# Performance work log

Measured on AMD Instinct MI355X. Metric: run time of the kernel, lower is better.

## Reference

```python
import jax, jax.numpy as jnp
import numpy as np

SEGMENT_LENGTHS = (768, 1536, 3072, 6144, 12288)
DILATED_RATIOS = (1, 2, 4, 8, 16)
NUM_HEADS = 12
NEG_INF = -1e9


def _layer_norm(x, g, b, eps=1e-5):
    mu = jnp.mean(x, axis=-1, keepdims=True)
    var = jnp.mean((x - mu) ** 2, axis=-1, keepdims=True)
    return (x - mu) * jax.lax.rsqrt(var + eps) * g + b


def _dilated_branch(q, k, v, w, r):
    # q,k,v: (B, L, H, Dh); segment length w, dilation ratio r (w % r == 0)
    B, L, H, Dh = q.shape
    Lp = -(-L // w) * w
    n, m = Lp // w, w // r
    gsz = -(-H // r)  # head-group size (heads padded up to a multiple of r in LongNet)
    offs = jnp.arange(H) // gsz  # per-head token offset within each r-block
    oh = jax.nn.one_hot(offs, r, dtype=q.dtype)  # (H, r)

    def gather(t):
        t = jnp.pad(t, ((0, 0), (0, Lp - L), (0, 0), (0, 0)))
        t = t.reshape(B, n, m, r, H, Dh)  # segments of w = m blocks of r
        return jnp.einsum('bnmrhd,hr->bnmhd', t, oh)  # each head picks its offset

    qi, ki, vi = gather(q), gather(k), gather(v)
    s = jnp.einsum('bnihd,bnjhd->bnhij', qi * (Dh ** -0.5), ki)  # (B,n,H,m,m)
    lse = jax.scipy.special.logsumexp(s, axis=-1)  # (B,n,H,m)
    o = jnp.einsum('bnhij,bnjhd->bnihd', jax.nn.softmax(s, axis=-1), vi)
    # scatter back to dense token positions; uncovered slots get 0 / -inf lse
    o_full = jnp.einsum('bnmhd,hr->bnmrhd', o, oh).reshape(B, Lp, H, Dh)
    lse = jnp.transpose(lse, (0, 1, 3, 2))  # (B,n,m,H)
    lse_full = jnp.where(oh.T[None, None, None] > 0, lse[:, :, :, None, :], NEG_INF)
    lse_full = lse_full.reshape(B, Lp, H)
    return o_full[:, :L], lse_full[:, :L]


def _dilated_attention(q, k, v):
    outs, lses = [], []
    for w, r in zip(SEGMENT_LENGTHS, DILATED_RATIOS):
        o, l = _dilated_branch(q, k, v, w, r)
        outs.append(o)
        lses.append(l)
    lse = jnp.stack(lses)  # (n_branch, B, L, H)
    wts = jnp.exp(lse - lse.max(0))
    wts = wts / wts.sum(0)  # softmax-combine branches by their lse (LongNet recombination)
    return (jnp.stack(outs) * wts[..., None]).sum(0)  # (B, L, H, Dh)


def _forward(x, patch_w, patch_b, cls_token, pos_embed,
             ln1_g, ln1_b, wq, bq, wk, bk, wv, bv, wo, bo,
             ln2_g, ln2_b, w1, b1, w2, b2, normf_g, normf_b, head_w, head_b):
    B, Cin, D, Hs, Ws = x.shape
    E = patch_w.shape[0]
    pd, ph, pw = patch_w.shape[2], patch_w.shape[3], patch_w.shape[4]
    # non-overlapping 3D patch embed (Conv3d with stride == kernel)
    xp = x.reshape(B, Cin, D // pd, pd, Hs // ph, ph, Ws // pw, pw)
    tok = jnp.einsum('bcxpyqzr,ecpqr->bxyze', xp, patch_w).reshape(B, -1, E) + patch_b
    tok = tok + pos_embed[:, 1:]
    cls = cls_token + pos_embed[:, :1]
    h = jnp.concatenate([jnp.broadcast_to(cls, (B, 1, E)), tok], axis=1)
    L = h.shape[1]
    Dh = E // NUM_HEADS
    depth = wq.shape[0]
    for i in range(depth):  # pre-LN transformer layers with LongNet dilated attention
        hn = _layer_norm(h, ln1_g[i], ln1_b[i])
        q = (hn @ wq[i] + bq[i]).reshape(B, L, NUM_HEADS, Dh)
        k = (hn @ wk[i] + bk[i]).reshape(B, L, NUM_HEADS, Dh)
        v = (hn @ wv[i] + bv[i]).reshape(B, L, NUM_HEADS, Dh)
        a = _dilated_attention(q, k, v).reshape(B, L, E)
        h = h + a @ wo[i] + bo[i]
        hn = _layer_norm(h, ln2_g[i], ln2_b[i])
        h = h + jax.nn.gelu(hn @ w1[i] + b1[i], approximate=False) @ w2[i] + b2[i]
    h = _layer_norm(h, normf_g, normf_b)
    return h[:, 0] @ head_w + head_b  # (B, num_classes)


def setup_inputs() -> dict:
    key = jax.random.key(0)
    ks = jax.random.split(key, 12)
    B, E, depth, ncls = 2, 768, 2, 1000
    D, Hs, Ws = 48, 256, 256
    N = (D // 4) * (Hs // 16) * (Ws // 16)  # 3072 patches
    f32 = jnp.float32
    s = 0.02
    return {
        'x': jax.random.normal(ks[0], (B, 1, D, Hs, Ws), f32),
        'patch_w': jax.random.normal(ks[1], (E, 1, 4, 16, 16), f32) * s,
        'patch_b': jnp.zeros((E,), f32),
        'cls_token': jax.random.normal(ks[2], (1, 1, E), f32) * s,
        'pos_embed': jax.random.normal(ks[3], (1, N + 1, E), f32) * s,
        'ln1_g': jnp.ones((depth, E), f32),
        'ln1_b': jnp.zeros((depth, E), f32),
        'wq': jax.random.normal(ks[4], (depth, E, E), f32) * s,
        'bq': jnp.zeros((depth, E), f32),
        'wk': jax.random.normal(ks[5], (depth, E, E), f32) * s,
        'bk': jnp.zeros((depth, E), f32),
        'wv': jax.random.normal(ks[6], (depth, E, E), f32) * s,
        'bv': jnp.zeros((depth, E), f32),
        'wo': jax.random.normal(ks[7], (depth, E, E), f32) * s,
        'bo': jnp.zeros((depth, E), f32),
        'ln2_g': jnp.ones((depth, E), f32),
        'ln2_b': jnp.zeros((depth, E), f32),
        'w1': jax.random.normal(ks[8], (depth, E, 4 * E), f32) * s,
        'b1': jnp.zeros((depth, 4 * E), f32),
        'w2': jax.random.normal(ks[9], (depth, 4 * E, E), f32) * s,
        'b2': jnp.zeros((depth, E), f32),
        'normf_g': jnp.ones((E,), f32),
        'normf_b': jnp.zeros((E,), f32),
        'head_w': jax.random.normal(ks[10], (E, ncls), f32) * s,
        'head_b': jnp.zeros((ncls,), f32),
    }


def reference(x, patch_w, patch_b, cls_token, pos_embed,
              ln1_g, ln1_b, wq, bq, wk, bk, wv, bv, wo, bo,
              ln2_g, ln2_b, w1, b1, w2, b2, normf_g, normf_b, head_w, head_b):
    return _forward(x, patch_w, patch_b, cls_token, pos_embed,
                    ln1_g, ln1_b, wq, bq, wk, bk, wv, bv, wo, bo,
                    ln2_g, ln2_b, w1, b1, w2, b2, normf_g, normf_b, head_w, head_b)
```

## Files before the change

kernel.cpp:

```cpp
#include <hip/hip_runtime.h>
#include <math.h>

#define TOK_L 3073
#define EMB 768
#define NH 12
#define DH 64
#define BATCH 2
#define QKVS 2304
#define HSZ ((size_t)BATCH * TOK_L * EMB)
#define MHC ((size_t)BATCH * TOK_L * NH)

typedef __bf16 bf16;
typedef __bf16 v8bf __attribute__((ext_vector_type(8)));
typedef __bf16 v4bf __attribute__((ext_vector_type(4)));
typedef float  v4f  __attribute__((ext_vector_type(4)));
typedef unsigned int v4u __attribute__((ext_vector_type(4)));

__device__ __forceinline__ v8bf zero8() {
    v8bf v;
    #pragma unroll
    for (int i = 0; i < 8; i++) v[i] = (bf16)0.f;
    return v;
}
__device__ __forceinline__ v4f zero4() {
    v4f v; v[0] = 0.f; v[1] = 0.f; v[2] = 0.f; v[3] = 0.f; return v;
}
__device__ __forceinline__ float gelu_f(float x) {
    return 0.5f * x * (1.0f + erff(x * 0.70710678118654752f));
}
__device__ __forceinline__ void gload16(const bf16* g, bf16* l) {
    __builtin_amdgcn_global_load_lds(
        (const __attribute__((address_space(1))) void*)g,
        (__attribute__((address_space(3))) void*)l, 16, 0, 0);
}

__device__ __forceinline__ void convT_tile(const float* __restrict__ src,
                                           bf16* __restrict__ dst,
                                           int K, int N, int tx, int ty)
{
    __shared__ float t[32][33];
    int n0 = tx * 32, k0 = ty * 32;
    int r = threadIdx.x >> 3, c4 = (threadIdx.x & 7) * 4;
    float4 v = *(const float4*)(src + (size_t)(k0 + r) * N + n0 + c4);
    t[r][c4 + 0] = v.x; t[r][c4 + 1] = v.y; t[r][c4 + 2] = v.z; t[r][c4 + 3] = v.w;
    __syncthreads();
    v4bf o;
    o[0] = (bf16)t[c4 + 0][r]; o[1] = (bf16)t[c4 + 1][r];
    o[2] = (bf16)t[c4 + 2][r]; o[3] = (bf16)t[c4 + 3][r];
    *(v4bf*)(dst + (size_t)(n0 + r) * K + k0 + c4) = o;
}

__global__ __launch_bounds__(256) void prep_weights(
    const float* __restrict__ wq, const float* __restrict__ wk,
    const float* __restrict__ wv, const float* __restrict__ wo,
    const float* __restrict__ w1, const float* __restrict__ w2,
    const float* __restrict__ patch_w,
    bf16* __restrict__ qkv_t0, bf16* __restrict__ wo_t0,
    bf16* __restrict__ w1_t, bf16* __restrict__ w2_t, bf16* __restrict__ pw_b)
{
    int bid = blockIdx.x;
    if (bid >= 13824) {
        int i = ((bid - 13824) * 256 + threadIdx.x) * 4;
        float4 v = *(const float4*)(patch_w + i);
        v4bf o; o[0] = (bf16)v.x; o[1] = (bf16)v.y; o[2] = (bf16)v.z; o[3] = (bf16)v.w;
        *(v4bf*)(pw_b + i) = o;
        return;
    }
    int layer = bid / 6912, t = bid % 6912;
    if (t < 1728) {
        int m = t / 576, tt = t % 576;
        const float* src = (m == 0 ? wq : m == 1 ? wk : wv) + (size_t)layer * 589824;
        bf16* dst = qkv_t0 + (size_t)layer * QKVS * 768 + (size_t)m * 589824;
        convT_tile(src, dst, 768, 768, tt % 24, tt / 24);
    } else if (t < 2304) {
        int tt = t - 1728;
        convT_tile(wo + (size_t)layer * 589824, wo_t0 + (size_t)layer * 589824,
                   768, 768, tt % 24, tt / 24);
    } else if (t < 4608) {
        int tt = t - 2304;
        convT_tile(w1 + (size_t)layer * 2359296, w1_t + (size_t)layer * 2359296,
                   768, 3072, tt % 96, tt / 96);
    } else {
        int tt = t - 4608;
        convT_tile(w2 + (size_t)layer * 2359296, w2_t + (size_t)layer * 2359296,
                   3072, 768, tt % 24, tt / 24);
    }
}

__global__ __launch_bounds__(256) void prep_small(const float* __restrict__ bq,
    const float* __restrict__ bk, const float* __restrict__ bv, float* __restrict__ d,
    const float* __restrict__ cls, const float* __restrict__ pos, float* __restrict__ h)
{
    int i = blockIdx.x * 256 + threadIdx.x;
    if (i < 2 * QKVS) {
        int layer = i / QKVS, j = i % QKVS;
        const float* s = (j < 768) ? bq : (j < 1536) ? bk : bv;
        d[i] = s[(size_t)layer * 768 + (j & 767)];
    }
    if (i < 2 * 768) {
        int b = i / 768, e = i % 768;
        h[(size_t)b * TOK_L * EMB + e] = cls[e] + pos[e];
    }
}

__global__ __launch_bounds__(256) void gather_patches(const float* __restrict__ x,
                                                      bf16* __restrict__ Xp) {
    int p = blockIdx.x;
    int b = p / 3072, pp = p % 3072;
    int px = pp >> 8, py = (pp >> 4) & 15, pz = pp & 15;
    for (int k = threadIdx.x; k < 1024; k += 256) {
        int pd = k >> 8, ph = (k >> 4) & 15, pw = k & 15;
        size_t src = ((size_t)(b * 48 + px * 4 + pd)) * 65536
                   + (size_t)(py * 16 + ph) * 256 + (size_t)(pz * 16 + pw);
        Xp[(size_t)p * 1024 + k] = (bf16)x[src];
    }
}

__device__ __forceinline__ void remap_tile(int NX, int MY, int G, int& xo, int& yo)
{
    int id = blockIdx.x + NX * blockIdx.y;
    int nwg = NX * MY;
    int xcd = id & 7, j = id >> 3;
    int q = nwg >> 3, r = nwg & 7;
    int n = xcd * q + (xcd < r ? xcd : r) + j;
    int full = MY / G;
    int bpg = NX * G;
    int nf = full * bpg;
    if (n < nf) {
        int gi = n / bpg, w = n - gi * bpg;
        int xi = w / G;
        xo = xi; yo = gi * G + (w - xi * G);
    } else {
        int t = MY - full * G;
        int w = n - nf;
        int xi = w / t;
        xo = xi; yo = full * G + (w - xi * t);
    }
}

template<int BN>
__global__ __launch_bounds__(256) void gemm_bf16(
    const bf16* __restrict__ A, const bf16* __restrict__ Bt,
    const float* __restrict__ bias, float* __restrict__ Cf,
    bf16* __restrict__ Cb, int M, int N, int K, int flags,
    const float* __restrict__ pos, int G)
{
    __shared__ bf16 As[3][128 * 32];
    __shared__ bf16 Bs[3][BN * 32];
    const int tid = threadIdx.x;
    const int lane = tid & 63, wid = tid >> 6;
    const int ln15 = lane & 15, q4 = lane >> 4;
    int xo, yo;
    remap_tile(gridDim.x, gridDim.y, G, xo, yo);
    const int m0 = yo * 128, n0 = xo * BN;
    const int wm = (wid & 1) * 64, wn = (wid >> 1) * (BN / 2);
    const int srow = lane >> 2;
    const int schunk = (lane & 3) * 8;
    const int NF = BN / 32;

    v4f acc[4][NF];
    #pragma unroll
    for (int i = 0; i < 4; i++)
        #pragma unroll
        for (int j = 0; j < NF; j++) acc[i][j] = zero4();

    const int NT = K >> 5;
    auto stage = [&](int kt, int bi) {
        const int k0 = kt << 5;
        #pragma unroll
        for (int i = 0; i < 2; i++) {
            int rg = wid * 32 + i * 16;
            int gm = m0 + rg + srow; if (gm >= M) gm = M - 1;
            gload16(A + (size_t)gm * K + k0 + schunk, &As[bi][rg * 32]);
        }
        if (BN == 128) {
            #pragma unroll
            for (int i = 0; i < 2; i++) {
                int rg = wid * 32 + i * 16;
                gload16(Bt + (size_t)(n0 + rg + srow) * K + k0 + schunk, &Bs[bi][rg * 32]);
            }
        } else {
            int rg = wid * 16;
            gload16(Bt + (size_t)(n0 + rg + srow) * K + k0 + schunk, &Bs[bi][rg * 32]);
        }
    };

    stage(0, 0);
    if (NT > 1) stage(1, 1);

    int cur = 0;
    for (int kt = 0; kt < NT; kt++) {
        int nx2 = cur + 2; if (nx2 >= 3) nx2 -= 3;
        if (kt + 2 < NT) {
            stage(kt + 2, nx2);
            if (BN == 128) asm volatile("s_waitcnt vmcnt(8)" ::: "memory");
            else           asm volatile("s_waitcnt vmcnt(6)" ::: "memory");
        } else if (kt + 1 < NT) {
            if (BN == 128) asm volatile("s_waitcnt vmcnt(4)" ::: "memory");
            else           asm volatile("s_waitcnt vmcnt(3)" ::: "memory");
        } else {
            asm volatile("s_waitcnt vmcnt(0)" ::: "memory");
        }
        __builtin_amdgcn_sched_barrier(0);
        __builtin_amdgcn_s_barrier();

        v8bf af[4], bfr[NF];
        #pragma unroll
        for (int mt = 0; mt < 4; mt++)
            af[mt] = *(const v8bf*)(&As[cur][(wm + mt * 16 + ln15) * 32 + q4 * 8]);
        #pragma unroll
        for (int nt = 0; nt < NF; nt++)
            bfr[nt] = *(const v8bf*)(&Bs[cur][(wn + nt * 16 + ln15) * 32 + q4 * 8]);
        #pragma unroll
        for (int mt = 0; mt < 4; mt++)
            #pragma unroll
            for (int nt = 0; nt < NF; nt++)
                acc[mt][nt] = __builtin_amdgcn_mfma_f32_16x16x32_bf16(af[mt], bfr[nt], acc[mt][nt], 0, 0, 0);
        __builtin_amdgcn_s_barrier();
        cur = cur + 1 == 3 ? 0 : cur + 1;
    }
    #pragma unroll
    for (int mt = 0; mt < 4; mt++) {
        #pragma unroll
        for (int nt = 0; nt < NF; nt++) {
            #pragma unroll
            for (int g = 0; g < 4; g++) {
                int row = m0 + wm + mt * 16 + q4 * 4 + g;
                if (row >= M) continue;
                int col = n0 + wn + nt * 16 + ln15;
                float v = acc[mt][nt][g] + bias[col];
                if (flags & 2) v = gelu_f(v);
                size_t crow;
                if (flags & 4) {
                    int rowp = row % 3072;
                    crow = (size_t)(row + row / 3072 + 1);
                    v += pos[(size_t)(rowp + 1) * EMB + col];
                } else crow = (size_t)row;
                size_t ci = crow * (size_t)N + col;
                if (flags & 8) Cb[ci] = (bf16)v;
                else { if (flags & 1) v += Cf[ci]; Cf[ci] = v; }
            }
        }
    }
}

__global__ __launch_bounds__(256) void layernorm_kernel(
    const float* __restrict__ x, const float* __restrict__ g,
    const float* __restrict__ bb, bf16* __restrict__ y, int nrows)
{
    int row = blockIdx.x;
    if (row >= nrows) return;
    int tid = threadIdx.x;
    const float* xr = x + (size_t)row * EMB;
    float v0 = xr[tid], v1 = xr[tid + 256], v2 = xr[tid + 512];
    __shared__ float red[256];
    red[tid] = v0 + v1 + v2;
    __syncthreads();
    for (int o = 128; o > 0; o >>= 1) { if (tid < o) red[tid] += red[tid + o]; __syncthreads(); }
    float mu = red[0] * (1.f / 768.f);
    __syncthreads();
    float d0 = v0 - mu, d1 = v1 - mu, d2 = v2 - mu;
    red[tid] = d0 * d0 + d1 * d1 + d2 * d2;
    __syncthreads();
    for (int o = 128; o > 0; o >>= 1) { if (tid < o) red[tid] += red[tid + o]; __syncthreads(); }
    float rs = rsqrtf(red[0] * (1.f / 768.f) + 1e-5f);
    bf16* yr = y + (size_t)row * EMB;
    yr[tid]       = (bf16)(d0 * rs * g[tid]       + bb[tid]);
    yr[tid + 256] = (bf16)(d1 * rs * g[tid + 256] + bb[tid + 256]);
    yr[tid + 512] = (bf16)(d2 * rs * g[tid + 512] + bb[tid + 512]);
}

__global__ __launch_bounds__(256) void pack_vt(const bf16* __restrict__ qkv,
                                               bf16* __restrict__ Vt)
{
    __shared__ bf16 t[64 * 65];
    int yy = blockIdx.y;
    int br, seg;
    if (yy < 5)       { br = 0; seg = yy; }
    else if (yy < 8)  { br = 1; seg = yy - 5; }
    else if (yy < 10) { br = 2; seg = yy - 8; }
    else if (yy == 10){ br = 3; seg = 0; }
    else              { br = 4; seg = 0; }
    const int r = 1 << br, w = 768 << br;
    const int gsz = (NH + r - 1) / r;
    const int bh = blockIdx.z;
    const int b = bh / NH, hd = bh % NH;
    const int off = hd / gsz;
    const int kbase = seg * w + off;
    const int kt = blockIdx.x;
    const int tid = threadIdx.x;
    const int dq = (tid & 7) * 8;
    #pragma unroll
    for (int p = 0; p < 2; p++) {
        int jl = (tid >> 3) + p * 32;
        int pk = kbase + (kt * 64 + jl) * r;
        v8bf val = (pk < TOK_L)
            ? *(const v8bf*)(qkv + (size_t)(b * TOK_L + pk) * QKVS + 1536 + hd * DH + dq)
            : zero8();
        #pragma unroll
        for (int i = 0; i < 8; i++) t[jl * 65 + dq + i] = val[i];
    }
    __syncthreads();
    #pragma unroll
    for (int p = 0; p < 2; p++) {
        int d = (tid >> 3) + p * 32;
        int kk = (tid & 7) * 8;
        v8bf o;
        #pragma unroll
        for (int i = 0; i < 8; i++) o[i] = t[(kk + i) * 65 + d];
        *(v8bf*)(Vt + ((size_t)(yy * 24 + bh) * 64 + d) * 768 + kt * 64 + kk) = o;
    }
}

__global__ __launch_bounds__(256) void attn_mfma(
    const bf16* __restrict__ qkv, const bf16* __restrict__ Vt,
    bf16* __restrict__ oac, bf16* __restrict__ obr, float* __restrict__ lse5)
{
    __shared__ bf16 kl[2 * 4096];
    const int tid = threadIdx.x;
    const int lane = tid & 63, wid = tid >> 6;
    const int ln15 = lane & 15, q4 = lane >> 4;
    const int bid = blockIdx.x;
    const int xcd = bid & 7, rest = bid >> 3;
    const int slot = rest / 6, t = rest - slot * 6;
    const int g = (slot << 3) | xcd;
    const int yy = g / 24, bh = g - yy * 24;
    int br, seg;
    if (yy < 5)       { br = 0; seg = yy; }
    else if (yy < 8)  { br = 1; seg = yy - 5; }
    else if (yy < 10) { br = 2; seg = yy - 8; }
    else if (yy == 10){ br = 3; seg = 0; }
    else              { br = 4; seg = 0; }
    const int r = 1 << br, w = 768 << br;
    const int gsz = (NH + r - 1) / r;
    const int b = bh / NH, hd = bh % NH;
    const int off = hd / gsz;
    const int sbase = seg * w + off;
    if (sbase + (t * 128) * r >= TOK_L) return;

    int n_valid = (TOK_L - sbase + r - 1) / r;
    if (n_valid > 768) n_valid = 768;
    const int kt_lim = (n_valid + 63) >> 6;
    const float pad_add = (float)(768 - n_valid);
    const int qoff = t * 128 + wid * 32;
    const bool wactive = (sbase + qoff * r) < TOK_L;

    const bf16* qb_ = qkv + hd * DH;
    const bf16* kb_ = qkv + 768 + hd * DH;

    const int swz = (ln15 & 7) * 8;

    auto stageK = [&](int ktv, int bufi) {
        #pragma unroll
        for (int p = 0; p < 2; p++) {
            int row = (tid >> 3) + p * 32;
            int pk = sbase + (ktv * 64 + row) * r;
            if (pk >= TOK_L) pk = 0;
            int colsw = ((tid & 7) ^ ((tid >> 3) & 7)) * 8;
            gload16(kb_ + (size_t)(b * TOK_L + pk) * QKVS + colsw,
                    kl + bufi * 4096 + wid * 512 + p * 2048);
        }
    };

    v8bf qf[2][2];
    #pragma unroll
    for (int mt = 0; mt < 2; mt++) {
        int pq = sbase + (qoff + mt * 16 + ln15) * r;
        #pragma unroll
        for (int ks = 0; ks < 2; ks++) {
            v8bf qv = (pq < TOK_L)
                ? *(const v8bf*)(qb_ + (size_t)(b * TOK_L + pq) * QKVS + ks * 32 + q4 * 8)
                : zero8();
            #pragma unroll
            for (int i = 0; i < 8; i++) qv[i] = (bf16)((float)qv[i] * 0.125f);
            qf[mt][ks] = qv;
        }
    }
    v4f o[2][4];
    float lsum[2];
    #pragma unroll
    for (int mt = 0; mt < 2; mt++) {
        lsum[mt] = 0.f;
        #pragma unroll
        for (int dt = 0; dt < 4; dt++) o[mt][dt] = zero4();
    }

    const bf16* vtb = Vt + (size_t)(yy * 24 + bh) * 64 * 768;

    stageK(0, 0);
    __syncthreads();

    for (int kt = 0; kt < kt_lim; kt++) {
        const int cur = kt & 1;
        if (kt + 1 < kt_lim) stageK(kt + 1, cur ^ 1);
        if (wactive) {
            const bf16* klc = kl + cur * 4096;
            v8bf kf[4][2];
            #pragma unroll
            for (int nt = 0; nt < 4; nt++)
                #pragma unroll
                for (int ks = 0; ks < 2; ks++)
                    kf[nt][ks] = *(const v8bf*)(klc + (nt * 16 + ln15) * 64
                                                + ((ks * 32 + q4 * 8) ^ swz));
            unsigned int paw[2][2][4];
            #pragma unroll
            for (int mt = 0; mt < 2; mt++) {
                v4f s[4];
                #pragma unroll
                for (int nt = 0; nt < 4; nt++) {
                    s[nt] = __builtin_amdgcn_mfma_f32_16x16x32_bf16(kf[nt][0], qf[mt][0], zero4(), 0, 0, 0);
                    s[nt] = __builtin_amdgcn_mfma_f32_16x16x32_bf16(kf[nt][1], qf[mt][1], s[nt], 0, 0, 0);
                }
                unsigned int W[4][2];
                float ls = 0.f;
                #pragma unroll
                for (int nt = 0; nt < 4; nt++) {
                    int kb = kt * 64 + nt * 16 + q4 * 4;
                    float p0 = (kb + 0 < n_valid) ? __expf(s[nt][0]) : 0.f;
                    float p1 = (kb + 1 < n_valid) ? __expf(s[nt][1]) : 0.f;
                    float p2 = (kb + 2 < n_valid) ? __expf(s[nt][2]) : 0.f;
                    float p3 = (kb + 3 < n_valid) ? __expf(s[nt][3]) : 0.f;
                    ls += (p0 + p1) + (p2 + p3);
                    asm("v_cvt_pk_bf16_f32 %0, %1, %2" : "=v"(W[nt][0]) : "v"(p0), "v"(p1));
                    asm("v_cvt_pk_bf16_f32 %0, %1, %2" : "=v"(W[nt][1]) : "v"(p2), "v"(p3));
                }
                lsum[mt] += ls;
                #pragma unroll
                for (int ks = 0; ks < 2; ks++) {
                    #pragma unroll
                    for (int h = 0; h < 2; h++) {
                        unsigned int a = W[2 * ks][h], c = W[2 * ks + 1][h];
                        asm("v_permlane32_swap_b32 %0, %1" : "+v"(a), "+v"(c));
                        asm("v_permlane16_swap_b32 %0, %1" : "+v"(a), "+v"(c));
                        paw[mt][ks][h]     = a;
                        paw[mt][ks][2 + h] = c;
                    }
                }
            }
            #pragma unroll
            for (int ks = 0; ks < 2; ks++) {
                v8bf vf[4];
                #pragma unroll
                for (int dt = 0; dt < 4; dt++)
                    vf[dt] = *(const v8bf*)(vtb + (size_t)(dt * 16 + ln15) * 768 + kt * 64 + ks * 32 + q4 * 8);
                #pragma unroll
                for (int mt = 0; mt < 2; mt++) {
                    v4u pw = { paw[mt][ks][0], paw[mt][ks][1], paw[mt][ks][2], paw[mt][ks][3] };
                    v8bf pa = __builtin_bit_cast(v8bf, pw);
                    #pragma unroll
                    for (int dt = 0; dt < 4; dt++)
                        o[mt][dt] = __builtin_amdgcn_mfma_f32_16x16x32_bf16(pa, vf[dt], o[mt][dt], 0, 0, 0);
                }
            }
        }
        __syncthreads();
    }
    if (!wactive) return;

    float lf[2];
    #pragma unroll
    for (int mt = 0; mt < 2; mt++) {
        float l = lsum[mt];
        l += __shfl_xor(l, 16, 64);
        l += __shfl_xor(l, 32, 64);
        l += pad_add;
        lf[mt] = l;
        if (q4 == 0) {
            int pq = sbase + (qoff + mt * 16 + ln15) * r;
            if (pq < TOK_L)
                lse5[(size_t)br * MHC + (size_t)(b * TOK_L + pq) * NH + hd] = __logf(l);
        }
    }

    bf16* od = (br == 0) ? oac : obr + (size_t)(br - 1) * HSZ;
    #pragma unroll
    for (int mt = 0; mt < 2; mt++) {
        #pragma unroll
        for (int g2 = 0; g2 < 4; g2++) {
            float l = __shfl(lf[mt], q4 * 4 + g2, 64);
            int row = mt * 16 + q4 * 4 + g2;
            int pq = sbase + (qoff + row) * r;
            if (pq >= TOK_L) continue;
            float linv = 1.f / l;
            #pragma unroll
            for (int dt = 0; dt < 4; dt++)
                od[(size_t)(b * TOK_L + pq) * EMB + hd * DH + dt * 16 + ln15] =
                    (bf16)(o[mt][dt][g2] * linv);
        }
    }
}

__global__ __launch_bounds__(256) void attn_combine(
    const bf16* __restrict__ oac, const bf16* __restrict__ obr,
    const float* __restrict__ lse5, bf16* __restrict__ outb)
{
    size_t e = (size_t)blockIdx.x * 256 + threadIdx.x;
    if (e >= HSZ) return;
    size_t g = e >> 6;
    int h = (int)(g % NH);
    int p = (int)((g / NH) % TOK_L);
    float l0 = lse5[g];
    float m = l0;
    float lv[4];
    bool cov[4];
    #pragma unroll
    for (int j = 0; j < 4; j++) {
        int r = 2 << j;
        int gsz = (NH + r - 1) / r;
        cov[j] = ((p & (r - 1)) == (h / gsz));
        if (cov[j]) {
            lv[j] = lse5[(size_t)(j + 1) * MHC + g];
            m = fmaxf(m, lv[j]);
        }
    }
    float w0 = __expf(l0 - m);
    float wsum = w0;
    float acc = w0 * (float)oac[e];
    #pragma unroll
    for (int j = 0; j < 4; j++) {
        if (cov[j]) {
            float wj = __expf(lv[j] - m);
            wsum += wj;
            acc = fmaf(wj, (float)obr[(size_t)j * HSZ + e], acc);
        }
    }
    outb[e] = (bf16)(acc / wsum);
}

__global__ __launch_bounds__(256) void head_kernel(
    const bf16* __restrict__ hn, const float* __restrict__ hw,
    const float* __restrict__ hb, float* __restrict__ out)
{
    int b = blockIdx.y;
    int c = blockIdx.x * 256 + threadIdx.x;
    __shared__ float srow[EMB];
    for (int e = threadIdx.x; e < EMB; e += 256)
        srow[e] = (float)hn[(size_t)b * TOK_L * EMB + e];
    __syncthreads();
    if (c < 1000) {
        float acc = hb[c];
        for (int e = 0; e < EMB; e++)
            acc = fmaf(srow[e], hw[(size_t)e * 1000 + c], acc);
        out[b * 1000 + c] = acc;
    }
}

extern "C" void kernel_launch(void* const* d_in, const int* in_sizes, int n_in,
                              void* d_out, int out_size, void* d_ws, size_t ws_size,
                              hipStream_t stream)
{
    const float* x       = (const float*)d_in[0];
    const float* patch_w = (const float*)d_in[1];
    const float* patch_b = (const float*)d_in[2];
    const float* cls_tok = (const float*)d_in[3];
    const float* pos_emb = (const float*)d_in[4];
    const float* ln1_g   = (const float*)d_in[5];
    const float* ln1_b   = (const float*)d_in[6];
    const float* wq      = (const float*)d_in[7];
    const float* bq      = (const float*)d_in[8];
    const float* wk      = (const float*)d_in[9];
    const float* bk      = (const float*)d_in[10];
    const float* wv      = (const float*)d_in[11];
    const float* bv      = (const float*)d_in[12];
    const float* wo      = (const float*)d_in[13];
    const float* bo      = (const float*)d_in[14];
    const float* ln2_g   = (const float*)d_in[15];
    const float* ln2_b   = (const float*)d_in[16];
    const float* w1      = (const float*)d_in[17];
    const float* b1      = (const float*)d_in[18];
    const float* w2      = (const float*)d_in[19];
    const float* b2      = (const float*)d_in[20];
    const float* normf_g = (const float*)d_in[21];
    const float* normf_b = (const float*)d_in[22];
    const float* head_w  = (const float*)d_in[23];
    const float* head_b  = (const float*)d_in[24];
    float* out = (float*)d_out;

    char* wp = (char*)d_ws;
    auto alloc = [&](size_t bytes) { char* r = wp; wp += (bytes + 255) & ~(size_t)255; return r; };
    float* h    = (float*)alloc(HSZ * 4);
    bf16*  hn   = (bf16*)alloc(HSZ * 2);
    bf16*  QKV  = (bf16*)alloc((size_t)BATCH * TOK_L * QKVS * 2);
    bf16*  oac  = (bf16*)alloc(HSZ * 2);
    float* lse5 = (float*)alloc(5 * MHC * 4);
    bf16*  Vt   = (bf16*)alloc((size_t)12 * 24 * 64 * 768 * 2);
    bf16*  mid  = (bf16*)alloc(4 * HSZ * 2);
    bf16*  obr  = mid;
    bf16*  Xp   = mid;

    bf16*  qkv_t0 = (bf16*)alloc((size_t)2 * QKVS * 768 * 2);
    bf16*  wo_t0  = (bf16*)alloc((size_t)2 * 768 * 768 * 2);
    bf16*  w1_t   = (bf16*)alloc((size_t)2 * 3072 * 768 * 2);
    bf16*  w2_t   = (bf16*)alloc((size_t)2 * 768 * 3072 * 2);
    bf16*  pw_b   = (bf16*)alloc((size_t)768 * 1024 * 2);
    float* bqkv   = (float*)alloc((size_t)2 * QKVS * 4);

    const int M = BATCH * TOK_L;
    const int MT = (M + 127) / 128;

    prep_weights<<<dim3(14592), 256, 0, stream>>>(wq, wk, wv, wo, w1, w2, patch_w,
                                                  qkv_t0, wo_t0, w1_t, w2_t, pw_b);
    prep_small<<<dim3(18), 256, 0, stream>>>(bq, bk, bv, bqkv, cls_tok, pos_emb, h);

    gather_patches<<<dim3(BATCH * 3072), 256, 0, stream>>>(x, Xp);
    gemm_bf16<64><<<dim3(12, 48), 256, 0, stream>>>(Xp, pw_b, patch_b, h, nullptr,
                                                    BATCH * 3072, 768, 1024, 4, pos_emb, 8);

    for (int layer = 0; layer < 2; layer++) {
        size_t bOff  = (size_t)layer * 768;
        size_t b1Off = (size_t)layer * 3072;
        bf16* qt   = qkv_t0 + (size_t)layer * QKVS * 768;
        bf16* wo_t = wo_t0 + (size_t)layer * 589824;

        layernorm_kernel<<<dim3(M), 256, 0, stream>>>(h, ln1_g + bOff, ln1_b + bOff, hn, M);
        gemm_bf16<128><<<dim3(18, MT), 256, 0, stream>>>(hn, qt, bqkv + (size_t)layer * QKVS,
                                                         nullptr, QKV, M, QKVS, 768, 8, nullptr, 8);

        pack_vt<<<dim3(12, 12, 24), 256, 0, stream>>>(QKV, Vt);
        attn_mfma<<<dim3(1728), 256, 0, stream>>>(QKV, Vt, oac, obr, lse5);
        attn_combine<<<dim3((unsigned)((HSZ + 255) / 256)), 256, 0, stream>>>(oac, obr, lse5, hn);

        gemm_bf16<64><<<dim3(12, MT), 256, 0, stream>>>(hn, wo_t, bo + bOff, h, nullptr,
                                                        M, 768, 768, 1, nullptr, 8);

        layernorm_kernel<<<dim3(M), 256, 0, stream>>>(h, ln2_g + bOff, ln2_b + bOff, hn, M);
        gemm_bf16<128><<<dim3(24, MT), 256, 0, stream>>>(hn, w1_t + (size_t)layer * 2359296, b1 + b1Off,
                                                         nullptr, mid, M, 3072, 768, 8 | 2, nullptr, 8);
        gemm_bf16<64><<<dim3(12, MT), 256, 0, stream>>>(mid, w2_t + (size_t)layer * 2359296, b2 + bOff,
                                                        h, nullptr, M, 768, 3072, 1, nullptr, 4);
    }

    layernorm_kernel<<<dim3(M), 256, 0, stream>>>(h, normf_g, normf_b, hn, M);
    head_kernel<<<dim3(4, BATCH), 256, 0, stream>>>(hn, head_w, head_b, out);
}
```

Baseline: 969.9 us.

## Add 256x256-tile 512-thread GEMM with quadrant-staged pipeline for QKV and FC1

Introduces a new GEMM kernel using 256x256 output tiles, 8 waves, a 4-slot swizzled LDS ring (128 KB), and a schedule that interleaves staging of the next K-tiles between four MFMA quadrant phases with priority raising. It replaces the 128-tile GEMM for the QKV projection and the FC1+GELU projection. Larger tiles raise data reuse per load and cut global traffic, at the cost of high register and LDS use, fewer workgroups (tail-wave imbalance with M≈6146), and many barriers per K step.

```diff
diff --git a/kernel.cpp b/kernel.cpp
--- a/kernel.cpp
+++ b/kernel.cpp
@@ -135,6 +135,149 @@
         int w = n - nf;
         int xi = w / t;
         xo = xi; yo = full * G + (w - xi * t);
+    }
+}
+
+__global__ __launch_bounds__(512, 2) void gemm256(
+    const bf16* __restrict__ A, const bf16* __restrict__ Bt,
+    const float* __restrict__ bias, bf16* __restrict__ Cb,
+    int M, int N, int K, int dogelu, int G)
+{
+    __shared__ bf16 AB[65536];
+    const int tid = threadIdx.x;
+    const int lane = tid & 63, wid = tid >> 6;
+    const int ln15 = lane & 15, q4 = lane >> 4;
+    int xo, yo;
+    remap_tile(gridDim.x, gridDim.y, G, xo, yo);
+    const int m0 = yo * 256, n0 = xo * 256;
+    const int wm = (wid & 1) * 128, wn = (wid >> 1) * 64;
+    const int srow = wid * 8 + (lane >> 3);
+    const int schunk = ((lane & 7) ^ ((lane >> 3) & 7)) * 8;
+    const int NT = K >> 6;
+
+    auto stageA = [&](int t, int h) {
+        const int slot = (2 * t + h) & 3;
+        bf16* dstb = AB + slot * 8192 + wid * 512;
+        const int k0 = t << 6;
+        #pragma unroll
+        for (int i = 0; i < 2; i++) {
+            int gm = m0 + h * 128 + i * 64 + srow; if (gm >= M) gm = M - 1;
+            gload16(A + (size_t)gm * K + k0 + schunk, dstb + i * 4096);
+        }
+    };
+    auto stageB = [&](int t, int h) {
+        const int slot = (2 * t + h) & 3;
+        bf16* dstb = AB + 32768 + slot * 8192 + wid * 512;
+        const int k0 = t << 6;
+        #pragma unroll
+        for (int i = 0; i < 2; i++) {
+            int gn = n0 + h * 128 + i * 64 + srow;
+            gload16(Bt + (size_t)gn * K + k0 + schunk, dstb + i * 4096);
+        }
+    };
+    auto rdA = [&](int kt, int mt, int ks) -> v8bf {
+        int R = wm + mt * 16 + ln15;
+        int slot = (2 * kt + (R >> 7)) & 3;
+        int r7 = R & 127;
+        return *(const v8bf*)(AB + slot * 8192 + r7 * 64 + ((ks * 4 + q4) ^ (r7 & 7)) * 8);
+    };
+    auto rdB = [&](int kt, int nt, int ks) -> v8bf {
+        int C = wn + nt * 16 + ln15;
+        int slot = (2 * kt + (C >> 7)) & 3;
+        int c7 = C & 127;
+        return *(const v8bf*)(AB + 32768 + slot * 8192 + c7 * 64 + ((ks * 4 + q4) ^ (c7 & 7)) * 8);
+    };
+
+    v4f acc[8][4];
+    #pragma unroll
+    for (int i = 0; i < 8; i++)
+        #pragma unroll
+        for (int j = 0; j < 4; j++) acc[i][j] = zero4();
+
+    stageA(0, 0); stageA(0, 1); stageB(0, 0); stageB(0, 1);
+    if (NT > 1) { stageA(1, 0); stageA(1, 1); }
+
+    v8bf af[8][2], bfr[4][2];
+    for (int kt = 0; kt < NT; kt++) {
+        if (kt + 1 < NT) {
+            stageB(kt + 1, 0);
+            asm volatile("s_waitcnt vmcnt(6)" ::: "memory");
+        } else {
+            asm volatile("s_waitcnt vmcnt(0)" ::: "memory");
+        }
+        __builtin_amdgcn_sched_barrier(0);
+        __builtin_amdgcn_s_barrier();
+        __builtin_amdgcn_sched_barrier(0);
+        #pragma unroll
+        for (int mt = 0; mt < 4; mt++) { af[mt][0] = rdA(kt, mt, 0); af[mt][1] = rdA(kt, mt, 1); }
+        #pragma unroll
+        for (int nt = 0; nt < 2; nt++) { bfr[nt][0] = rdB(kt, nt, 0); bfr[nt][1] = rdB(kt, nt, 1); }
+        __builtin_amdgcn_s_setprio(1);
+        #pragma unroll
+        for (int mt = 0; mt < 4; mt++)
+            #pragma unroll
+            for (int nt = 0; nt < 2; nt++)
+                #pragma unroll
+                for (int ks = 0; ks < 2; ks++)
+                    acc[mt][nt] = __builtin_amdgcn_mfma_f32_16x16x32_bf16(af[mt][ks], bfr[nt][ks], acc[mt][nt], 0, 0, 0);
+        __builtin_amdgcn_s_setprio(0);
+        __builtin_amdgcn_s_barrier();
+        #pragma unroll
+        for (int mt = 4; mt < 8; mt++) { af[mt][0] = rdA(kt, mt, 0); af[mt][1] = rdA(kt, mt, 1); }
+        #pragma unroll
+        for (int nt = 2; nt < 4; nt++) { bfr[nt][0] = rdB(kt, nt, 0); bfr[nt][1] = rdB(kt, nt, 1); }
+        if (kt + 1 < NT) stageB(kt + 1, 1);
+        __builtin_amdgcn_s_barrier();
+        __builtin_amdgcn_s_setprio(1);
+        #pragma unroll
+        for (int mt = 0; mt < 4; mt++)
+            #pragma unroll
+            for (int nt = 2; nt < 4; nt++)
+                #pragma unroll
+                for (int ks = 0; ks < 2; ks++)
+                    acc[mt][nt] = __builtin_amdgcn_mfma_f32_16x16x32_bf16(af[mt][ks], bfr[nt][ks], acc[mt][nt], 0, 0, 0);
+        __builtin_amdgcn_s_setprio(0);
+        __builtin_amdgcn_s_barrier();
+        if (kt + 2 < NT) stageA(kt + 2, 0);
+        __builtin_amdgcn_s_barrier();
+        __builtin_amdgcn_s_setprio(1);
+        #pragma unroll
+        for (int mt = 4; mt < 8; mt++)
+            #pragma unroll
+            for (int nt = 2; nt < 4; nt++)
+                #pragma unroll
+                for (int ks = 0; ks < 2; ks++)
+                    acc[mt][nt] = __builtin_amdgcn_mfma_f32_16x16x32_bf16(af[mt][ks], bfr[nt][ks], acc[mt][nt], 0, 0, 0);
+        __builtin_amdgcn_s_setprio(0);
+        __builtin_amdgcn_s_barrier();
+        if (kt + 2 < NT) stageA(kt + 2, 1);
+        __builtin_amdgcn_s_barrier();
+        __builtin_amdgcn_s_setprio(1);
+        #pragma unroll
+        for (int mt = 4; mt < 8; mt++)
+            #pragma unroll
+            for (int nt = 0; nt < 2; nt++)
+                #pragma unroll
+                for (int ks = 0; ks < 2; ks++)
+                    acc[mt][nt] = __builtin_amdgcn_mfma_f32_16x16x32_bf16(af[mt][ks], bfr[nt][ks], acc[mt][nt], 0, 0, 0);
+        __builtin_amdgcn_s_setprio(0);
+        __builtin_amdgcn_s_barrier();
+    }
+
+    #pragma unroll
+    for (int mt = 0; mt < 8; mt++) {
+        #pragma unroll
+        for (int nt = 0; nt < 4; nt++) {
+            #pragma unroll
+            for (int g = 0; g < 4; g++) {
+                int row = m0 + wm + mt * 16 + q4 * 4 + g;
+                if (row >= M) continue;
+                int col = n0 + wn + nt * 16 + ln15;
+                float v = acc[mt][nt][g] + bias[col];
+                if (dogelu) v = gelu_f(v);
+                Cb[(size_t)row * N + col] = (bf16)v;
+            }
+        }
     }
 }
 
@@ -597,6 +740,7 @@
 
     const int M = BATCH * TOK_L;
     const int MT = (M + 127) / 128;
+    const int MT2 = (M + 255) / 256;
 
     prep_weights<<<dim3(14592), 256, 0, stream>>>(wq, wk, wv, wo, w1, w2, patch_w,
                                                   qkv_t0, wo_t0, w1_t, w2_t, pw_b);
@@ -613,8 +757,8 @@
         bf16* wo_t = wo_t0 + (size_t)layer * 589824;
 
         layernorm_kernel<<<dim3(M), 256, 0, stream>>>(h, ln1_g + bOff, ln1_b + bOff, hn, M);
-        gemm_bf16<128><<<dim3(18, MT), 256, 0, stream>>>(hn, qt, bqkv + (size_t)layer * QKVS,
-                                                         nullptr, QKV, M, QKVS, 768, 8, nullptr, 8);
+        gemm256<<<dim3(9, MT2), 512, 0, stream>>>(hn, qt, bqkv + (size_t)layer * QKVS,
+                                                  QKV, M, QKVS, 768, 0, 4);
 
         pack_vt<<<dim3(12, 12, 24), 256, 0, stream>>>(QKV, Vt);
         attn_mfma<<<dim3(1728), 256, 0, stream>>>(QKV, Vt, oac, obr, lse5);
@@ -624,8 +768,8 @@
                                                         M, 768, 768, 1, nullptr, 8);
 
         layernorm_kernel<<<dim3(M), 256, 0, stream>>>(h, ln2_g + bOff, ln2_b + bOff, hn, M);
-        gemm_bf16<128><<<dim3(24, MT), 256, 0, stream>>>(hn, w1_t + (size_t)layer * 2359296, b1 + b1Off,
-                                                         nullptr, mid, M, 3072, 768, 8 | 2, nullptr, 8);
+        gemm256<<<dim3(12, MT2), 512, 0, stream>>>(hn, w1_t + (size_t)layer * 2359296, b1 + b1Off,
+                                                   mid, M, 3072, 768, 1, 4);
         gemm_bf16<64><<<dim3(12, MT), 256, 0, stream>>>(mid, w2_t + (size_t)layer * 2359296, b2 + bOff,
                                                         h, nullptr, M, 768, 3072, 1, nullptr, 4);
     }
```

New measurement: 1.000 ms. 3.1% more time.
